# Performance work log

Measured on AMD Instinct MI355X. Metric: run time of the kernel, lower is better.

## Reference

```python
import jax, jax.numpy as jnp
import numpy as np

N_NODES = 5000
N_EDGES = 50000
BATCH = 8
SEQ = 12
IN_CH = 2
HID = 64
OUT_CH = 1
K = 3
N_LAYERS = 2


def setup_inputs() -> dict:
    key = jax.random.key(0)
    ks = jax.random.split(key, 20)
    d = {}
    d["x"] = jax.random.normal(ks[0], (BATCH, SEQ, N_NODES, IN_CH), dtype=jnp.float32)
    d["edge_index"] = jax.random.randint(ks[1], (2, N_EDGES), 0, N_NODES, dtype=jnp.int32)

    def w(k, fin):
        return jax.random.normal(k, (2, K, fin, HID), dtype=jnp.float32) * 0.05

    fins = [IN_CH + HID, HID + HID]
    i = 2
    for l in range(N_LAYERS):
        for g in ("z", "r", "h"):
            d["W" + g + str(l)] = w(ks[i], fins[l]); i += 1
            d["b" + g + str(l)] = jnp.zeros((HID,), jnp.float32)
    d["Wo"] = jax.random.normal(ks[i], (HID, OUT_CH), dtype=jnp.float32) * 0.05
    d["bo"] = jnp.zeros((OUT_CH,), jnp.float32)
    return d


def reference(x, edge_index,
              Wz0, bz0, Wr0, br0, Wh0, bh0,
              Wz1, bz1, Wr1, br1, Wh1, bh1,
              Wo, bo):
    B, T, N, _ = x.shape
    src, dst = edge_index[0], edge_index[1]
    ones = jnp.ones(src.shape, x.dtype)
    deg_out = jax.ops.segment_sum(ones, src, num_segments=N)
    deg_in = jax.ops.segment_sum(ones, dst, num_segments=N)
    inv = lambda dgr: jnp.where(dgr > 0, 1.0 / dgr, 0.0)
    norm_out = inv(deg_out)[src]  # [E], 1/deg_out(src)
    norm_in = inv(deg_in)[dst]    # [E], 1/deg_in(dst)

    def prop(X, norm):
        # X: [N, B, F] -> sparse matvec via gather/scatter
        msg = norm[:, None, None] * X[src]
        return jax.ops.segment_sum(msg, dst, num_segments=N)

    def dconv(X, W, b):
        # X: [N, B, Fin]; W: [2, K, Fin, H]; dual-direction Chebyshev diffusion
        H = jnp.einsum('nbf,fh->nbh', X, W[0, 0] + W[1, 0])
        Tx0o = Tx0i = X
        Tx1o = prop(X, norm_out)
        Tx1i = prop(X, norm_in)
        H = H + jnp.einsum('nbf,fh->nbh', Tx1o, W[0, 1]) \
              + jnp.einsum('nbf,fh->nbh', Tx1i, W[1, 1])
        for k in range(2, W.shape[1]):
            Tx2o = 2.0 * prop(Tx1o, norm_out) - Tx0o
            Tx2i = 2.0 * prop(Tx1i, norm_in) - Tx0i
            H = H + jnp.einsum('nbf,fh->nbh', Tx2o, W[0, k]) \
                  + jnp.einsum('nbf,fh->nbh', Tx2i, W[1, k])
            Tx0o, Tx1o = Tx1o, Tx2o
            Tx0i, Tx1i = Tx1i, Tx2i
        return H + b

    def cell(Xin, H, p):
        Wz, bz, Wr, br, Wh, bh = p
        XH = jnp.concatenate([Xin, H], axis=-1)
        Z = jax.nn.sigmoid(dconv(XH, Wz, bz))
        R = jax.nn.sigmoid(dconv(XH, Wr, br))
        Ht = jnp.tanh(dconv(jnp.concatenate([Xin, H * R], axis=-1), Wh, bh))
        return Z * H + (1.0 - Z) * Ht

    layers = [(Wz0, bz0, Wr0, br0, Wh0, bh0), (Wz1, bz1, Wr1, br1, Wh1, bh1)]
    hid = Wo.shape[0]
    h0 = jnp.zeros((len(layers), N, B, hid), x.dtype)
    xs = jnp.transpose(x, (1, 2, 0, 3))  # [T, N, B, F]

    def step(h, xt):
        inp = xt
        new_h = []
        for l, p in enumerate(layers):
            hl = cell(inp, h[l], p)
            new_h.append(hl)
            inp = hl
        h = jnp.stack(new_h)
        out = jnp.einsum('nbh,ho->nbo', h[-1], Wo) + bo
        return h, out

    _, outs = jax.lax.scan(step, h0, xs)      # [T, N, B, O]
    return jnp.transpose(outs, (2, 0, 1, 3))  # [B, T, N, O]
```

## Files before the change

kernel.cpp:

```cpp
#include <hip/hip_runtime.h>
#include <math.h>

#define NNODES 5000
#define NEDGES 50000
#define SEQT 12
#define NB 40000
#define MAXDEG 128

typedef __attribute__((ext_vector_type(8))) _Float16 half8;
typedef __attribute__((ext_vector_type(2))) _Float16 half2v;
typedef __attribute__((ext_vector_type(4))) float f32x4;


__global__ void count_deg_k(const int* __restrict__ ei, int* deg_out, int* deg_in){
    int e = blockIdx.x*blockDim.x + threadIdx.x;
    if (e < NEDGES){
        atomicAdd(&deg_out[ei[e]], 1);
        atomicAdd(&deg_in[ei[NEDGES + e]], 1);
    }
}

__global__ void scan_k(const int* __restrict__ deg_in, int* __restrict__ row_ptr){
    __shared__ int part[256];
    int tid = threadIdx.x;
    int base = tid*20;
    int loc[20]; int s = 0;
    for (int i=0;i<20;i++){
        int idx = base+i;
        int v = (idx < NNODES) ? deg_in[idx] : 0;
        loc[i] = s; s += v;
    }
    part[tid] = s;
    __syncthreads();
    for (int off=1; off<256; off<<=1){
        int v = (tid>=off) ? part[tid-off] : 0;
        __syncthreads();
        part[tid] += v;
        __syncthreads();
    }
    int prev = (tid==0) ? 0 : part[tid-1];
    for (int i=0;i<20;i++){
        int idx = base+i;
        if (idx < NNODES) row_ptr[idx] = prev + loc[i];
    }
    if (tid==255) row_ptr[NNODES] = part[255];
}

__global__ void fill_csr_k(const int* __restrict__ ei, const int* __restrict__ deg_out,
                           const int* __restrict__ deg_in, const int* __restrict__ row_ptr,
                           int* cursor, int* __restrict__ csr_src,
                           float* __restrict__ csr_wo, float* __restrict__ csr_wi){
    int e = blockIdx.x*blockDim.x + threadIdx.x;
    if (e >= NEDGES) return;
    int s = ei[e], d = ei[NEDGES+e];
    int pos = atomicAdd(&cursor[d], 1);
    int slot = row_ptr[d] + pos;
    csr_src[slot] = s;
    csr_wo[slot] = 1.f/(float)deg_out[s];
    csr_wi[slot] = 1.f/(float)deg_in[d];
}

__global__ void prepack_x_k(const float* __restrict__ x, _Float16* __restrict__ Xtph){
    int idx = blockIdx.x*256 + threadIdx.x;
    if (idx >= SEQT*NB*2) return;
    int tt = idx / (NB*2);
    int r2 = idx - tt*(NB*2);
    int row = r2 >> 1, f = r2 & 1;
    int n = row >> 3, b = row & 7;
    Xtph[idx] = (_Float16)x[((size_t)(b*SEQT+tt)*NNODES + n)*2 + f];
}

__device__ __forceinline__ float wfetch(const float* __restrict__ W, int F, int slot, int f, int c){
    const float* p0 = W + ((size_t)0*F + f)*64 + c;
    const float* p1 = W + ((size_t)1*F + f)*64 + c;
    const float* p2 = W + ((size_t)2*F + f)*64 + c;
    const float* p3 = W + ((size_t)3*F + f)*64 + c;
    const float* p4 = W + ((size_t)4*F + f)*64 + c;
    const float* p5 = W + ((size_t)5*F + f)*64 + c;
    switch(slot){
        case 0: return *p0 + *p3 - *p2 - *p5;
        case 1: return *p1;
        case 2: return *p4;
        case 3: return 2.f * *p2;
        default: return 2.f * *p5;
    }
}

__global__ void pack_l0_k(const float* __restrict__ W, _Float16* __restrict__ wh){
    int idx = blockIdx.x*256 + threadIdx.x;
    if (idx >= 4*11*64) return;
    int lane = idx & 63, rest = idx >> 6;
    int ks = rest % 11, cf = rest / 11;
    int col = cf*16 + (lane & 15);
    int kb = ks*32 + ((lane>>4)<<3);
    size_t o = ((size_t)(ks*4 + cf)*64 + lane)*8;
    for (int j=0;j<8;j++){
        int k = kb + j;
        float v = 0.f;
        if (ks == 0){
            if (k < 10) v = wfetch(W, 66, k>>1, k&1, col);
        } else {
            int slot = (ks-1)>>1;
            int f = 2 + k - 32 - 64*slot;
            v = wfetch(W, 66, slot, f, col);
        }
        wh[o+j] = (_Float16)v;
    }
}

__global__ void pack_l1_k(const float* __restrict__ W, _Float16* __restrict__ wh){
    int idx = blockIdx.x*256 + threadIdx.x;
    if (idx >= 4*20*64) return;
    int lane = idx & 63, rest = idx >> 6;
    int ks = rest % 20, cf = rest / 20;
    int col = cf*16 + (lane & 15);
    int kb = ks*32 + ((lane>>4)<<3);
    int slot = ks >> 2;
    size_t o = ((size_t)(ks*4 + cf)*64 + lane)*8;
    for (int j=0;j<8;j++){
        int k = kb + j;
        int f = k - slot*128;
        wh[o+j] = (_Float16)wfetch(W, 128, slot, f, col);
    }
}


template<int WH>
__global__ __launch_bounds__(WH) void k_dualh(
    const _Float16* __restrict__ S,
    _Float16* __restrict__ Yo, _Float16* __restrict__ Yi,
    const int* __restrict__ rp, const int* __restrict__ cs,
    const float* __restrict__ cwo, const float* __restrict__ cwi){
    constexpr int SLAB = 8*WH;
    int n = blockIdx.x;
    int beg = rp[n], deg = rp[n+1]-beg;
    int nst = deg < MAXDEG ? deg : MAXDEG;
    __shared__ int s_o[MAXDEG]; __shared__ float swo[MAXDEG], swi[MAXDEG];
    for (int j=threadIdx.x; j<nst; j+=WH){
        s_o[j] = cs[beg+j]*SLAB;
        swo[j] = cwo[beg+j]; swi[j] = cwi[beg+j];
    }
    __syncthreads();
    int off = threadIdx.x*8;
    float ao[8] = {0,0,0,0,0,0,0,0}, ai[8] = {0,0,0,0,0,0,0,0};
    for (int j=0;j<nst;j++){
        half8 v = *(const half8*)(S + s_o[j] + off);
        float wo=swo[j], wi=swi[j];
        #pragma unroll
        for (int e=0;e<8;e++){
            float xv = (float)v[e];
            ao[e]=fmaf(wo,xv,ao[e]); ai[e]=fmaf(wi,xv,ai[e]);
        }
    }
    for (int j=nst;j<deg;j++){
        half8 v = *(const half8*)(S + (size_t)cs[beg+j]*SLAB + off);
        float wo=cwo[beg+j], wi=cwi[beg+j];
        #pragma unroll
        for (int e=0;e<8;e++){
            float xv = (float)v[e];
            ao[e]=fmaf(wo,xv,ao[e]); ai[e]=fmaf(wi,xv,ai[e]);
        }
    }
    half8 po, pi;
    #pragma unroll
    for (int e=0;e<8;e++){ po[e]=(_Float16)ao[e]; pi[e]=(_Float16)ai[e]; }
    *(half8*)(Yo + (size_t)n*SLAB + off) = po;
    *(half8*)(Yi + (size_t)n*SLAB + off) = pi;
}

template<int WH>
__global__ __launch_bounds__(WH) void k_prop2h(
    const _Float16* __restrict__ T1o, const _Float16* __restrict__ T1i,
    _Float16* __restrict__ U2o, _Float16* __restrict__ U2i,
    const int* __restrict__ rp, const int* __restrict__ cs,
    const float* __restrict__ cwo, const float* __restrict__ cwi){
    constexpr int SLAB = 8*WH;
    int bx = blockIdx.x;
    int n = bx >> 1, sel = bx & 1;
    const _Float16* S = sel ? T1i : T1o;
    _Float16* U = sel ? U2i : U2o;
    const float* cw = sel ? cwi : cwo;
    int beg = rp[n], deg = rp[n+1]-beg;
    int nst = deg < MAXDEG ? deg : MAXDEG;
    __shared__ int s_o[MAXDEG]; __shared__ float s_w[MAXDEG];
    for (int j=threadIdx.x; j<nst; j+=WH){
        s_o[j] = cs[beg+j]*SLAB;
        s_w[j] = cw[beg+j];
    }
    __syncthreads();
    int off = threadIdx.x*8;
    float a[8] = {0,0,0,0,0,0,0,0};
    for (int j=0;j<nst;j++){
        half8 v = *(const half8*)(S + s_o[j] + off);
        float w=s_w[j];
        #pragma unroll
        for (int e=0;e<8;e++) a[e]=fmaf(w,(float)v[e],a[e]);
    }
    for (int j=nst;j<deg;j++){
        half8 v = *(const half8*)(S + (size_t)cs[beg+j]*SLAB + off);
        float w=cw[beg+j];
        #pragma unroll
        for (int e=0;e<8;e++) a[e]=fmaf(w,(float)v[e],a[e]);
    }
    half8 p;
    #pragma unroll
    for (int e=0;e<8;e++) p[e]=(_Float16)a[e];
    *(half8*)(U + (size_t)n*SLAB + off) = p;
}

__global__ __launch_bounds__(64) void k_dual_l0zrh(
    const _Float16* __restrict__ h0h, const _Float16* __restrict__ Xt,
    _Float16* __restrict__ T1o, _Float16* __restrict__ T1i, _Float16* __restrict__ XTh,
    const int* __restrict__ rp, const int* __restrict__ cs,
    const float* __restrict__ cwo, const float* __restrict__ cwi){
    int n = blockIdx.x;
    int beg = rp[n], deg = rp[n+1]-beg;
    int nst = deg < MAXDEG ? deg : MAXDEG;
    __shared__ int s_o[MAXDEG]; __shared__ float swo[MAXDEG], swi[MAXDEG];
    for (int j=threadIdx.x; j<nst; j+=64){
        s_o[j] = cs[beg+j]*512;
        swo[j] = cwo[beg+j]; swi[j] = cwi[beg+j];
    }
    __syncthreads();
    int off = threadIdx.x*8;
    {
        float ao[8] = {0,0,0,0,0,0,0,0}, ai[8] = {0,0,0,0,0,0,0,0};
        for (int j=0;j<nst;j++){
            half8 v = *(const half8*)(h0h + s_o[j] + off);
            float wo=swo[j], wi=swi[j];
            #pragma unroll
            for (int e=0;e<8;e++){
                float xv = (float)v[e];
                ao[e]=fmaf(wo,xv,ao[e]); ai[e]=fmaf(wi,xv,ai[e]);
            }
        }
        for (int j=nst;j<deg;j++){
            half8 v = *(const half8*)(h0h + (size_t)cs[beg+j]*512 + off);
            float wo=cwo[beg+j], wi=cwi[beg+j];
            #pragma unroll
            for (int e=0;e<8;e++){
                float xv = (float)v[e];
                ao[e]=fmaf(wo,xv,ao[e]); ai[e]=fmaf(wi,xv,ai[e]);
            }
        }
        half8 po, pi;
        #pragma unroll
        for (int e=0;e<8;e++){ po[e]=(_Float16)ao[e]; pi[e]=(_Float16)ai[e]; }
        *(half8*)(T1o + (size_t)n*512 + off) = po;
        *(half8*)(T1i + (size_t)n*512 + off) = pi;
    }
    if (threadIdx.x < 8){
        int b = threadIdx.x;
        float ax0=0,ax1=0, ay0=0,ay1=0;
        for (int j=0;j<nst;j++){
            int src = s_o[j] >> 9;
            half2v v = *(const half2v*)(Xt + src*16 + b*2);
            float x0=(float)v[0], x1=(float)v[1];
            ax0=fmaf(swo[j],x0,ax0); ax1=fmaf(swo[j],x1,ax1);
            ay0=fmaf(swi[j],x0,ay0); ay1=fmaf(swi[j],x1,ay1);
        }
        for (int j=nst;j<deg;j++){
            int src = cs[beg+j];
            half2v v = *(const half2v*)(Xt + src*16 + b*2);
            float x0=(float)v[0], x1=(float)v[1];
            ax0=fmaf(cwo[beg+j],x0,ax0); ax1=fmaf(cwo[beg+j],x1,ax1);
            ay0=fmaf(cwi[beg+j],x0,ay0); ay1=fmaf(cwi[beg+j],x1,ay1);
        }
        size_t ro = (size_t)(n*8 + b)*32;
        XTh[ro+0] = Xt[(size_t)(n*8+b)*2+0];
        XTh[ro+1] = Xt[(size_t)(n*8+b)*2+1];
        XTh[ro+2] = (_Float16)ax0; XTh[ro+3] = (_Float16)ax1;
        XTh[ro+4] = (_Float16)ay0; XTh[ro+5] = (_Float16)ay1;
    }
}

__global__ __launch_bounds__(64) void k_prop2_l0zrh(
    const _Float16* __restrict__ T1o, const _Float16* __restrict__ T1i,
    _Float16* __restrict__ T2o, _Float16* __restrict__ T2i, _Float16* __restrict__ XTh,
    const int* __restrict__ rp, const int* __restrict__ cs,
    const float* __restrict__ cwo, const float* __restrict__ cwi){
    int bx = blockIdx.x;
    int n = bx >> 1, sel = bx & 1;
    const _Float16* S = sel ? T1i : T1o;
    _Float16* U = sel ? T2i : T2o;
    const float* cw = sel ? cwi : cwo;
    int beg = rp[n], deg = rp[n+1]-beg;
    int nst = deg < MAXDEG ? deg : MAXDEG;
    __shared__ int s_o[MAXDEG]; __shared__ float s_w[MAXDEG];
    for (int j=threadIdx.x; j<nst; j+=64){
        s_o[j] = cs[beg+j]*512;
        s_w[j] = cw[beg+j];
    }
    __syncthreads();
    int off = threadIdx.x*8;
    {
        float a[8] = {0,0,0,0,0,0,0,0};
        for (int j=0;j<nst;j++){
            half8 v = *(const half8*)(S + s_o[j] + off);
            float w=s_w[j];
            #pragma unroll
            for (int e=0;e<8;e++) a[e]=fmaf(w,(float)v[e],a[e]);
        }
        for (int j=nst;j<deg;j++){
            half8 v = *(const half8*)(S + (size_t)cs[beg+j]*512 + off);
            float w=cw[beg+j];
            #pragma unroll
            for (int e=0;e<8;e++) a[e]=fmaf(w,(float)v[e],a[e]);
        }
        half8 p;
        #pragma unroll
        for (int e=0;e<8;e++) p[e]=(_Float16)a[e];
        *(half8*)(U + (size_t)n*512 + off) = p;
    }
    if (threadIdx.x < 8){
        int b = threadIdx.x;
        int xo = 2 + 2*sel;
        float a0=0,a1=0;
        for (int j=0;j<nst;j++){
            int src = s_o[j] >> 9;
            half2v v = *(const half2v*)(XTh + (size_t)src*256 + b*32 + xo);
            a0=fmaf(s_w[j],(float)v[0],a0); a1=fmaf(s_w[j],(float)v[1],a1);
        }
        for (int j=nst;j<deg;j++){
            int src = cs[beg+j];
            half2v v = *(const half2v*)(XTh + (size_t)src*256 + b*32 + xo);
            a0=fmaf(cw[beg+j],(float)v[0],a0); a1=fmaf(cw[beg+j],(float)v[1],a1);
        }
        size_t ro = (size_t)(n*8 + b)*32 + 6 + 2*sel;
        XTh[ro+0] = (_Float16)a0; XTh[ro+1] = (_Float16)a1;
    }
}

__global__ __launch_bounds__(128) void k_dual2x64h(
    const _Float16* __restrict__ h0h, const _Float16* __restrict__ h1h,
    _Float16* __restrict__ T1o, _Float16* __restrict__ T1i,
    const int* __restrict__ rp, const int* __restrict__ cs,
    const float* __restrict__ cwo, const float* __restrict__ cwi){
    int n = blockIdx.x;
    int beg = rp[n], deg = rp[n+1]-beg;
    int nst = deg < MAXDEG ? deg : MAXDEG;
    __shared__ int s_o[MAXDEG]; __shared__ float swo[MAXDEG], swi[MAXDEG];
    for (int j=threadIdx.x; j<nst; j+=128){
        s_o[j] = cs[beg+j]*512;
        swo[j] = cwo[beg+j]; swi[j] = cwi[beg+j];
    }
    __syncthreads();
    int off = threadIdx.x*8;
    int b = off >> 7, c = off & 127;
    const _Float16* S = (c < 64) ? h0h : h1h;
    int soff = b*64 + (c & 63);
    float ao[8] = {0,0,0,0,0,0,0,0}, ai[8] = {0,0,0,0,0,0,0,0};
    for (int j=0;j<nst;j++){
        half8 v = *(const half8*)(S + s_o[j] + soff);
        float wo=swo[j], wi=swi[j];
        #pragma unroll
        for (int e=0;e<8;e++){
            float xv = (float)v[e];
            ao[e]=fmaf(wo,xv,ao[e]); ai[e]=fmaf(wi,xv,ai[e]);
        }
    }
    for (int j=nst;j<deg;j++){
        half8 v = *(const half8*)(S + (size_t)cs[beg+j]*512 + soff);
        float wo=cwo[beg+j], wi=cwi[beg+j];
        #pragma unroll
        for (int e=0;e<8;e++){
            float xv = (float)v[e];
            ao[e]=fmaf(wo,xv,ao[e]); ai[e]=fmaf(wi,xv,ai[e]);
        }
    }
    half8 po, pi;
    #pragma unroll
    for (int e=0;e<8;e++){ po[e]=(_Float16)ao[e]; pi[e]=(_Float16)ai[e]; }
    *(half8*)(T1o + (size_t)n*1024 + off) = po;
    *(half8*)(T1i + (size_t)n*1024 + off) = pi;
}


struct KD { const _Float16* a; int st; };
struct GA { KD kd[20]; };

template<int NK, int NG, int EPI>
__global__ __launch_bounds__(256) void k_gemm(GA ga,
    const _Float16* __restrict__ wh0, const float* __restrict__ b0,
    const _Float16* __restrict__ wh1, const float* __restrict__ b1,
    float* __restrict__ Z, _Float16* __restrict__ Gout,
    float* __restrict__ Hf, _Float16* __restrict__ Hh,
    const float* __restrict__ Wo, const float* __restrict__ bo,
    float* __restrict__ out, int t){
    __shared__ _Float16 ldsb[2][NG*2048];
    __shared__ float spr[4][32];
    const int tid = threadIdx.x;
    const int lane = tid & 63, wv = tid >> 6, rl = lane & 15, kg = lane >> 4;
    const int m0 = blockIdx.x*64 + (wv&1)*32;
    const int cfb = (wv>>1)*2;
    const _Float16* wsrc[2] = {wh0, wh1};

    half8 srg[NG];
    half8 a0, a1, a0n, a1n;

    auto sload = [&](int ks){
        #pragma unroll
        for (int j=0;j<NG;j++)
            srg[j] = *(const half8*)(wsrc[j] + (size_t)ks*2048 + tid*8);
    };
    auto swrite = [&](int buf){
        #pragma unroll
        for (int j=0;j<NG;j++)
            *(half8*)&ldsb[buf][j*2048 + tid*8] = srg[j];
    };
    auto aload = [&](int ks, half8& x0, half8& x1){
        const _Float16* base = ga.kd[ks].a;
        const int st = ga.kd[ks].st;
        x0 = *(const half8*)(base + (size_t)(m0+rl)*st + kg*8);
        x1 = *(const half8*)(base + (size_t)(m0+16+rl)*st + kg*8);
    };

    f32x4 acc[NG][2][2];
    #pragma unroll
    for (int g=0; g<NG; ++g)
        #pragma unroll
        for (int cc=0; cc<2; ++cc)
            #pragma unroll
            for (int mr=0; mr<2; ++mr){
                acc[g][cc][mr][0]=0.f; acc[g][cc][mr][1]=0.f;
                acc[g][cc][mr][2]=0.f; acc[g][cc][mr][3]=0.f;
            }

    sload(0); swrite(0);
    if (NK>1) sload(1);
    aload(0, a0, a1);
    __syncthreads();
    for (int ks=0; ks<NK; ++ks){
        const int cur = ks & 1;
        if (ks+1 < NK){ swrite(cur^1); aload(ks+1, a0n, a1n); }
        if (ks+2 < NK) sload(ks+2);
        #pragma unroll
        for (int g=0; g<NG; ++g){
            #pragma unroll
            for (int cc=0; cc<2; ++cc){
                half8 bv = *(const half8*)&ldsb[cur][g*2048 + (cfb+cc)*512 + lane*8];
                acc[g][cc][0] = __builtin_amdgcn_mfma_f32_16x16x32_f16(a0, bv, acc[g][cc][0], 0, 0, 0);
                acc[g][cc][1] = __builtin_amdgcn_mfma_f32_16x16x32_f16(a1, bv, acc[g][cc][1], 0, 0, 0);
            }
        }
        __syncthreads();
        a0 = a0n; a1 = a1n;
    }

    if constexpr (EPI == 0){
        #pragma unroll
        for (int cc=0; cc<2; ++cc){
            const int col = (cfb+cc)*16 + rl;
            float bzv = b0[col], brv = b1[col];
            #pragma unroll
            for (int mr=0; mr<2; ++mr)
                #pragma unroll
                for (int i=0;i<4;i++){
                    int row = m0 + mr*16 + kg*4 + i;
                    float z = 1.f/(1.f+__expf(-(acc[0][cc][mr][i] + bzv)));
                    float r = 1.f/(1.f+__expf(-(acc[NG-1][cc][mr][i] + brv)));
                    size_t ix = (size_t)row*64 + col;
                    Z[ix] = z;
                    Gout[ix] = (_Float16)(Hf[ix]*r);
                }
        }
    } else {
        float pr[2][4] = {{0.f,0.f,0.f,0.f},{0.f,0.f,0.f,0.f}};
        #pragma unroll
        for (int cc=0; cc<2; ++cc){
            const int col = (cfb+cc)*16 + rl;
            float bv = b0[col];
            float wo_c = 0.f;
            if constexpr (EPI == 2) wo_c = Wo[col];
            #pragma unroll
            for (int mr=0; mr<2; ++mr)
                #pragma unroll
                for (int i=0;i<4;i++){
                    int row = m0 + mr*16 + kg*4 + i;
                    float ht = tanhf(acc[0][cc][mr][i] + bv);
                    size_t ix = (size_t)row*64 + col;
                    float z = Z[ix];
                    float hn = z*Hf[ix] + (1.f-z)*ht;
                    Hf[ix] = hn;
                    Hh[ix] = (_Float16)hn;
                    if constexpr (EPI == 2) pr[mr][i] = fmaf(hn, wo_c, pr[mr][i]);
                }
        }
        if constexpr (EPI == 2){
            #pragma unroll
            for (int mr=0; mr<2; ++mr)
                #pragma unroll
                for (int i=0;i<4;i++){
                    float v = pr[mr][i];
                    v += __shfl_xor(v, 1);
                    v += __shfl_xor(v, 2);
                    v += __shfl_xor(v, 4);
                    v += __shfl_xor(v, 8);
                    if (rl == 0) spr[wv][mr*16 + kg*4 + i] = v;
                }
            __syncthreads();
            if (tid < 64){
                int r = tid;
                float v = spr[r>>5][r&31] + spr[(r>>5)|2][r&31] + bo[0];
                int row = blockIdx.x*64 + r;
                int n = row >> 3, b = row & 7;
                out[(size_t)(b*SEQT + t)*NNODES + n] = v;
            }
        }
    }
}


extern "C" void kernel_launch(void* const* d_in, const int* in_sizes, int n_in,
                              void* d_out, int out_size, void* d_ws, size_t ws_size,
                              hipStream_t stream){
    (void)in_sizes; (void)n_in; (void)out_size; (void)ws_size;
    const float* x  = (const float*)d_in[0];
    const int*   ei = (const int*)d_in[1];
    const float* Wz[2] = {(const float*)d_in[2],  (const float*)d_in[8]};
    const float* bz[2] = {(const float*)d_in[3],  (const float*)d_in[9]};
    const float* Wr[2] = {(const float*)d_in[4],  (const float*)d_in[10]};
    const float* br[2] = {(const float*)d_in[5],  (const float*)d_in[11]};
    const float* Wh[2] = {(const float*)d_in[6],  (const float*)d_in[12]};
    const float* bh[2] = {(const float*)d_in[7],  (const float*)d_in[13]};
    const float* Wo = (const float*)d_in[14];
    const float* bo = (const float*)d_in[15];
    float* out = (float*)d_out;

    char* p = (char*)d_ws;
    auto alloc = [&](size_t bytes)->char*{
        char* r = p; p += (bytes + 255) & ~(size_t)255; return r;
    };
    const size_t H64  = (size_t)NB*64*2;
    const size_t H128 = (size_t)NB*128*2;
    const size_t F64  = (size_t)NB*64*4;

    _Float16* Xtph = (_Float16*)alloc((size_t)SEQT*NB*2*2);
    float*    h0f = (float*)alloc(F64);
    float*    h1f = (float*)alloc(F64);
    float*    Z0  = (float*)alloc(F64);
    float*    Z1  = (float*)alloc(F64);
    _Float16* h0h = (_Float16*)alloc(H64);
    _Float16* h1h = (_Float16*)alloc(H64);
    _Float16* XTh = (_Float16*)alloc((size_t)NB*32*2);
    _Float16* Th1o = (_Float16*)alloc(H64);
    _Float16* Th1i = (_Float16*)alloc(H64);
    _Float16* Th2o = (_Float16*)alloc(H64);
    _Float16* Th2i = (_Float16*)alloc(H64);
    _Float16* G0L0 = (_Float16*)alloc(H64);
    _Float16* G1o0 = (_Float16*)alloc(H64);
    _Float16* G1i0 = (_Float16*)alloc(H64);
    _Float16* G2o0 = (_Float16*)alloc(H64);
    _Float16* G2i0 = (_Float16*)alloc(H64);
    _Float16* T1o128 = (_Float16*)alloc(H128);
    _Float16* T1i128 = (_Float16*)alloc(H128);
    _Float16* U2o128 = (_Float16*)alloc(H128);
    _Float16* U2i128 = (_Float16*)alloc(H128);
    _Float16* G0p  = (_Float16*)alloc(H64);
    _Float16* G1o1 = (_Float16*)alloc(H64);
    _Float16* G1i1 = (_Float16*)alloc(H64);
    _Float16* G2o1 = (_Float16*)alloc(H64);
    _Float16* G2i1 = (_Float16*)alloc(H64);
    _Float16 *whl0[3], *whl1[3];
    for (int g=0; g<3; ++g){
        whl0[g] = (_Float16*)alloc((size_t)4*11*64*8*2);
        whl1[g] = (_Float16*)alloc((size_t)4*20*64*8*2);
    }
    int* deg_out = (int*)alloc(NNODES*4);
    int* deg_in  = (int*)alloc(NNODES*4);
    int* row_ptr = (int*)alloc((NNODES+1)*4);
    int* cursor  = (int*)alloc(NNODES*4);
    int* csr_src = (int*)alloc(NEDGES*4);
    float* csr_wo = (float*)alloc(NEDGES*4);
    float* csr_wi = (float*)alloc(NEDGES*4);

    hipMemsetAsync(deg_out, 0, NNODES*4, stream);
    hipMemsetAsync(deg_in,  0, NNODES*4, stream);
    hipMemsetAsync(cursor,  0, NNODES*4, stream);
    hipMemsetAsync(h0f, 0, F64, stream);
    hipMemsetAsync(h1f, 0, F64, stream);
    hipMemsetAsync(h0h, 0, H64, stream);
    hipMemsetAsync(h1h, 0, H64, stream);
    hipMemsetAsync(XTh, 0, (size_t)NB*32*2, stream);

    count_deg_k<<<(NEDGES+255)/256, 256, 0, stream>>>(ei, deg_out, deg_in);
    scan_k<<<1, 256, 0, stream>>>(deg_in, row_ptr);
    fill_csr_k<<<(NEDGES+255)/256, 256, 0, stream>>>(ei, deg_out, deg_in, row_ptr,
                                                     cursor, csr_src, csr_wo, csr_wi);
    prepack_x_k<<<(SEQT*NB*2+255)/256, 256, 0, stream>>>(x, Xtph);
    const float* Wptr0[3] = {Wz[0], Wr[0], Wh[0]};
    const float* Wptr1[3] = {Wz[1], Wr[1], Wh[1]};
    for (int g=0; g<3; ++g){
        pack_l0_k<<<(4*11*64+255)/256, 256, 0, stream>>>(Wptr0[g], whl0[g]);
        pack_l1_k<<<(4*20*64+255)/256, 256, 0, stream>>>(Wptr1[g], whl1[g]);
    }

    GA gaL0zr = {}, gaL0h = {}, gaL1zr = {}, gaL1h = {};
    {
        const _Float16* t64[5] = {h0h, Th1o, Th1i, Th2o, Th2i};
        gaL0zr.kd[0] = {XTh, 32};
        for (int s=0; s<5; ++s){
            gaL0zr.kd[1+2*s] = {t64[s], 64};
            gaL0zr.kd[2+2*s] = {t64[s]+32, 64};
        }
        const _Float16* g64[5] = {G0L0, G1o0, G1i0, G2o0, G2i0};
        gaL0h.kd[0] = {XTh, 32};
        for (int s=0; s<5; ++s){
            gaL0h.kd[1+2*s] = {g64[s], 64};
            gaL0h.kd[2+2*s] = {g64[s]+32, 64};
        }
        gaL1zr.kd[0] = {h0h, 64};    gaL1zr.kd[1] = {h0h+32, 64};
        gaL1zr.kd[2] = {h1h, 64};    gaL1zr.kd[3] = {h1h+32, 64};
        const _Float16* t128[4] = {T1o128, T1i128, U2o128, U2i128};
        for (int s=0; s<4; ++s)
            for (int q=0; q<4; ++q)
                gaL1zr.kd[4+4*s+q] = {t128[s]+32*q, 128};
        gaL1h.kd[0] = {h0h, 64};  gaL1h.kd[1] = {h0h+32, 64};
        gaL1h.kd[2] = {G0p, 64};  gaL1h.kd[3] = {G0p+32, 64};
        const _Float16* gh[4] = {G1o1, G1i1, G2o1, G2i1};
        for (int s=0; s<4; ++s){
            gaL1h.kd[4+4*s+0] = {t128[s], 128};
            gaL1h.kd[4+4*s+1] = {t128[s]+32, 128};
            gaL1h.kd[4+4*s+2] = {gh[s], 64};
            gaL1h.kd[4+4*s+3] = {gh[s]+32, 64};
        }
    }

    for (int t=0; t<SEQT; ++t){
        k_dual_l0zrh<<<NNODES, 64, 0, stream>>>(h0h, Xtph + (size_t)t*NB*2, Th1o, Th1i, XTh,
                                                row_ptr, csr_src, csr_wo, csr_wi);
        k_prop2_l0zrh<<<2*NNODES, 64, 0, stream>>>(Th1o, Th1i, Th2o, Th2i, XTh,
                                                row_ptr, csr_src, csr_wo, csr_wi);
        k_gemm<11,2,0><<<NB/64, 256, 0, stream>>>(gaL0zr,
            whl0[0], bz[0], whl0[1], br[0],
            Z0, G0L0, h0f, nullptr, nullptr, nullptr, nullptr, 0);
        k_dualh<64><<<NNODES, 64, 0, stream>>>(G0L0, G1o0, G1i0, row_ptr, csr_src, csr_wo, csr_wi);
        k_prop2h<64><<<2*NNODES, 64, 0, stream>>>(G1o0, G1i0, G2o0, G2i0,
                                                row_ptr, csr_src, csr_wo, csr_wi);
        k_gemm<11,1,1><<<NB/64, 256, 0, stream>>>(gaL0h,
            whl0[2], bh[0], nullptr, nullptr,
            Z0, nullptr, h0f, h0h, nullptr, nullptr, nullptr, 0);
        k_dual2x64h<<<NNODES, 128, 0, stream>>>(h0h, h1h, T1o128, T1i128,
                                                row_ptr, csr_src, csr_wo, csr_wi);
        k_prop2h<128><<<2*NNODES, 128, 0, stream>>>(T1o128, T1i128, U2o128, U2i128,
                                                row_ptr, csr_src, csr_wo, csr_wi);
        k_gemm<20,2,0><<<NB/64, 256, 0, stream>>>(gaL1zr,
            whl1[0], bz[1], whl1[1], br[1],
            Z1, G0p, h1f, nullptr, nullptr, nullptr, nullptr, 0);
        k_dualh<64><<<NNODES, 64, 0, stream>>>(G0p, G1o1, G1i1, row_ptr, csr_src, csr_wo, csr_wi);
        k_prop2h<64><<<2*NNODES, 64, 0, stream>>>(G1o1, G1i1, G2o1, G2i1,
                                                row_ptr, csr_src, csr_wo, csr_wi);
        k_gemm<20,1,2><<<NB/64, 256, 0, stream>>>(gaL1h,
            whl1[2], bh[1], nullptr, nullptr,
            Z1, nullptr, h1f, h1h, Wo, bo, out, t);
    }
}
```

Before: 2.409 ms.

## Unroll gather loops, merge dual-direction prop blocks, deepen GEMM A-prefetch queue

The sparse gather loops in the diffusion kernels are unrolled by four so several neighbour loads are in flight at once. The second-hop propagation kernels now run the out and in directions in one block of twice the width, so CSR indices and weights are staged into shared memory once per node instead of twice. The MFMA GEMM replaces its single-stage A-operand prefetch with a four-deep register queue to hide global load latency. The deeper queue and unrolling raise register pressure, which may reduce occupancy.

```diff
diff --git a/kernel.cpp b/kernel.cpp
--- a/kernel.cpp
+++ b/kernel.cpp
@@ -125,6 +125,16 @@
 }
 
 
+#define ACC8(vv, ww) { \
+    float _w = (ww); \
+    _Pragma("unroll") \
+    for (int e=0;e<8;e++) a[e]=fmaf(_w,(float)(vv)[e],a[e]); }
+#define ACC8D(vv, wo_, wi_) { \
+    float _wo = (wo_), _wi = (wi_); \
+    _Pragma("unroll") \
+    for (int e=0;e<8;e++){ float xv=(float)(vv)[e]; \
+        ao[e]=fmaf(_wo,xv,ao[e]); ai[e]=fmaf(_wi,xv,ai[e]); } }
+
 template<int WH>
 __global__ __launch_bounds__(WH) void k_dualh(
     const _Float16* __restrict__ S,
@@ -143,23 +153,24 @@
     __syncthreads();
     int off = threadIdx.x*8;
     float ao[8] = {0,0,0,0,0,0,0,0}, ai[8] = {0,0,0,0,0,0,0,0};
-    for (int j=0;j<nst;j++){
+    int j = 0;
+    for (; j+3<nst; j+=4){
+        half8 v0 = *(const half8*)(S + s_o[j]   + off);
+        half8 v1 = *(const half8*)(S + s_o[j+1] + off);
+        half8 v2 = *(const half8*)(S + s_o[j+2] + off);
+        half8 v3 = *(const half8*)(S + s_o[j+3] + off);
+        ACC8D(v0, swo[j],   swi[j]);
+        ACC8D(v1, swo[j+1], swi[j+1]);
+        ACC8D(v2, swo[j+2], swi[j+2]);
+        ACC8D(v3, swo[j+3], swi[j+3]);
+    }
+    for (; j<nst; ++j){
         half8 v = *(const half8*)(S + s_o[j] + off);
-        float wo=swo[j], wi=swi[j];
-        #pragma unroll
-        for (int e=0;e<8;e++){
-            float xv = (float)v[e];
-            ao[e]=fmaf(wo,xv,ao[e]); ai[e]=fmaf(wi,xv,ai[e]);
-        }
-    }
-    for (int j=nst;j<deg;j++){
+        ACC8D(v, swo[j], swi[j]);
+    }
+    for (j=nst; j<deg; ++j){
         half8 v = *(const half8*)(S + (size_t)cs[beg+j]*SLAB + off);
-        float wo=cwo[beg+j], wi=cwi[beg+j];
-        #pragma unroll
-        for (int e=0;e<8;e++){
-            float xv = (float)v[e];
-            ao[e]=fmaf(wo,xv,ao[e]); ai[e]=fmaf(wi,xv,ai[e]);
-        }
+        ACC8D(v, cwo[beg+j], cwi[beg+j]);
     }
     half8 po, pi;
     #pragma unroll
@@ -169,38 +180,42 @@
 }
 
 template<int WH>
-__global__ __launch_bounds__(WH) void k_prop2h(
+__global__ __launch_bounds__(2*WH) void k_prop2m(
     const _Float16* __restrict__ T1o, const _Float16* __restrict__ T1i,
     _Float16* __restrict__ U2o, _Float16* __restrict__ U2i,
     const int* __restrict__ rp, const int* __restrict__ cs,
     const float* __restrict__ cwo, const float* __restrict__ cwi){
     constexpr int SLAB = 8*WH;
-    int bx = blockIdx.x;
-    int n = bx >> 1, sel = bx & 1;
+    int n = blockIdx.x;
+    int beg = rp[n], deg = rp[n+1]-beg;
+    int nst = deg < MAXDEG ? deg : MAXDEG;
+    __shared__ int s_o[MAXDEG]; __shared__ float swo[MAXDEG], swi[MAXDEG];
+    for (int j=threadIdx.x; j<nst; j+=2*WH){
+        s_o[j] = cs[beg+j]*SLAB;
+        swo[j] = cwo[beg+j]; swi[j] = cwi[beg+j];
+    }
+    __syncthreads();
+    const int sel = (threadIdx.x >= WH);
     const _Float16* S = sel ? T1i : T1o;
     _Float16* U = sel ? U2i : U2o;
-    const float* cw = sel ? cwi : cwo;
-    int beg = rp[n], deg = rp[n+1]-beg;
-    int nst = deg < MAXDEG ? deg : MAXDEG;
-    __shared__ int s_o[MAXDEG]; __shared__ float s_w[MAXDEG];
-    for (int j=threadIdx.x; j<nst; j+=WH){
-        s_o[j] = cs[beg+j]*SLAB;
-        s_w[j] = cw[beg+j];
-    }
-    __syncthreads();
-    int off = threadIdx.x*8;
+    const float* sw = sel ? swi : swo;
+    int off = (threadIdx.x & (WH-1))*8;
     float a[8] = {0,0,0,0,0,0,0,0};
-    for (int j=0;j<nst;j++){
+    int j = 0;
+    for (; j+3<nst; j+=4){
+        half8 v0 = *(const half8*)(S + s_o[j]   + off);
+        half8 v1 = *(const half8*)(S + s_o[j+1] + off);
+        half8 v2 = *(const half8*)(S + s_o[j+2] + off);
+        half8 v3 = *(const half8*)(S + s_o[j+3] + off);
+        ACC8(v0, sw[j]); ACC8(v1, sw[j+1]); ACC8(v2, sw[j+2]); ACC8(v3, sw[j+3]);
+    }
+    for (; j<nst; ++j){
         half8 v = *(const half8*)(S + s_o[j] + off);
-        float w=s_w[j];
-        #pragma unroll
-        for (int e=0;e<8;e++) a[e]=fmaf(w,(float)v[e],a[e]);
-    }
-    for (int j=nst;j<deg;j++){
+        ACC8(v, sw[j]);
+    }
+    for (j=nst; j<deg; ++j){
         half8 v = *(const half8*)(S + (size_t)cs[beg+j]*SLAB + off);
-        float w=cw[beg+j];
-        #pragma unroll
-        for (int e=0;e<8;e++) a[e]=fmaf(w,(float)v[e],a[e]);
+        ACC8(v, sel ? cwi[beg+j] : cwo[beg+j]);
     }
     half8 p;
     #pragma unroll
@@ -225,23 +240,24 @@
     int off = threadIdx.x*8;
     {
         float ao[8] = {0,0,0,0,0,0,0,0}, ai[8] = {0,0,0,0,0,0,0,0};
-        for (int j=0;j<nst;j++){
+        int j = 0;
+        for (; j+3<nst; j+=4){
+            half8 v0 = *(const half8*)(h0h + s_o[j]   + off);
+            half8 v1 = *(const half8*)(h0h + s_o[j+1] + off);
+            half8 v2 = *(const half8*)(h0h + s_o[j+2] + off);
+            half8 v3 = *(const half8*)(h0h + s_o[j+3] + off);
+            ACC8D(v0, swo[j],   swi[j]);
+            ACC8D(v1, swo[j+1], swi[j+1]);
+            ACC8D(v2, swo[j+2], swi[j+2]);
+            ACC8D(v3, swo[j+3], swi[j+3]);
+        }
+        for (; j<nst; ++j){
             half8 v = *(const half8*)(h0h + s_o[j] + off);
-            float wo=swo[j], wi=swi[j];
-            #pragma unroll
-            for (int e=0;e<8;e++){
-                float xv = (float)v[e];
-                ao[e]=fmaf(wo,xv,ao[e]); ai[e]=fmaf(wi,xv,ai[e]);
-            }
-        }
-        for (int j=nst;j<deg;j++){
+            ACC8D(v, swo[j], swi[j]);
+        }
+        for (j=nst; j<deg; ++j){
             half8 v = *(const half8*)(h0h + (size_t)cs[beg+j]*512 + off);
-            float wo=cwo[beg+j], wi=cwi[beg+j];
-            #pragma unroll
-            for (int e=0;e<8;e++){
-                float xv = (float)v[e];
-                ao[e]=fmaf(wo,xv,ao[e]); ai[e]=fmaf(wi,xv,ai[e]);
-            }
+            ACC8D(v, cwo[beg+j], cwi[beg+j]);
         }
         half8 po, pi;
         #pragma unroll
@@ -274,57 +290,62 @@
     }
 }
 
-__global__ __launch_bounds__(64) void k_prop2_l0zrh(
+__global__ __launch_bounds__(128) void k_prop2_l0m(
     const _Float16* __restrict__ T1o, const _Float16* __restrict__ T1i,
     _Float16* __restrict__ T2o, _Float16* __restrict__ T2i, _Float16* __restrict__ XTh,
     const int* __restrict__ rp, const int* __restrict__ cs,
     const float* __restrict__ cwo, const float* __restrict__ cwi){
-    int bx = blockIdx.x;
-    int n = bx >> 1, sel = bx & 1;
+    int n = blockIdx.x;
+    int beg = rp[n], deg = rp[n+1]-beg;
+    int nst = deg < MAXDEG ? deg : MAXDEG;
+    __shared__ int s_o[MAXDEG]; __shared__ float swo[MAXDEG], swi[MAXDEG];
+    for (int j=threadIdx.x; j<nst; j+=128){
+        s_o[j] = cs[beg+j]*512;
+        swo[j] = cwo[beg+j]; swi[j] = cwi[beg+j];
+    }
+    __syncthreads();
+    const int sel = (threadIdx.x >= 64);
     const _Float16* S = sel ? T1i : T1o;
     _Float16* U = sel ? T2i : T2o;
-    const float* cw = sel ? cwi : cwo;
-    int beg = rp[n], deg = rp[n+1]-beg;
-    int nst = deg < MAXDEG ? deg : MAXDEG;
-    __shared__ int s_o[MAXDEG]; __shared__ float s_w[MAXDEG];
-    for (int j=threadIdx.x; j<nst; j+=64){
-        s_o[j] = cs[beg+j]*512;
-        s_w[j] = cw[beg+j];
-    }
-    __syncthreads();
-    int off = threadIdx.x*8;
+    const float* sw = sel ? swi : swo;
+    int off = (threadIdx.x & 63)*8;
     {
         float a[8] = {0,0,0,0,0,0,0,0};
-        for (int j=0;j<nst;j++){
+        int j = 0;
+        for (; j+3<nst; j+=4){
+            half8 v0 = *(const half8*)(S + s_o[j]   + off);
+            half8 v1 = *(const half8*)(S + s_o[j+1] + off);
+            half8 v2 = *(const half8*)(S + s_o[j+2] + off);
+            half8 v3 = *(const half8*)(S + s_o[j+3] + off);
+            ACC8(v0, sw[j]); ACC8(v1, sw[j+1]); ACC8(v2, sw[j+2]); ACC8(v3, sw[j+3]);
+        }
+        for (; j<nst; ++j){
             half8 v = *(const half8*)(S + s_o[j] + off);
-            float w=s_w[j];
-            #pragma unroll
-            for (int e=0;e<8;e++) a[e]=fmaf(w,(float)v[e],a[e]);
-        }
-        for (int j=nst;j<deg;j++){
+            ACC8(v, sw[j]);
+        }
+        for (j=nst; j<deg; ++j){
             half8 v = *(const half8*)(S + (size_t)cs[beg+j]*512 + off);
-            float w=cw[beg+j];
-            #pragma unroll
-            for (int e=0;e<8;e++) a[e]=fmaf(w,(float)v[e],a[e]);
+            ACC8(v, sel ? cwi[beg+j] : cwo[beg+j]);
         }
         half8 p;
         #pragma unroll
         for (int e=0;e<8;e++) p[e]=(_Float16)a[e];
         *(half8*)(U + (size_t)n*512 + off) = p;
     }
-    if (threadIdx.x < 8){
-        int b = threadIdx.x;
+    if ((threadIdx.x & 63) < 8){
+        int b = threadIdx.x & 7;
         int xo = 2 + 2*sel;
         float a0=0,a1=0;
         for (int j=0;j<nst;j++){
             int src = s_o[j] >> 9;
             half2v v = *(const half2v*)(XTh + (size_t)src*256 + b*32 + xo);
-            a0=fmaf(s_w[j],(float)v[0],a0); a1=fmaf(s_w[j],(float)v[1],a1);
+            a0=fmaf(sw[j],(float)v[0],a0); a1=fmaf(sw[j],(float)v[1],a1);
         }
         for (int j=nst;j<deg;j++){
             int src = cs[beg+j];
+            float w = sel ? cwi[beg+j] : cwo[beg+j];
             half2v v = *(const half2v*)(XTh + (size_t)src*256 + b*32 + xo);
-            a0=fmaf(cw[beg+j],(float)v[0],a0); a1=fmaf(cw[beg+j],(float)v[1],a1);
+            a0=fmaf(w,(float)v[0],a0); a1=fmaf(w,(float)v[1],a1);
         }
         size_t ro = (size_t)(n*8 + b)*32 + 6 + 2*sel;
         XTh[ro+0] = (_Float16)a0; XTh[ro+1] = (_Float16)a1;
@@ -350,23 +371,24 @@
     const _Float16* S = (c < 64) ? h0h : h1h;
     int soff = b*64 + (c & 63);
     float ao[8] = {0,0,0,0,0,0,0,0}, ai[8] = {0,0,0,0,0,0,0,0};
-    for (int j=0;j<nst;j++){
+    int j = 0;
+    for (; j+3<nst; j+=4){
+        half8 v0 = *(const half8*)(S + s_o[j]   + soff);
+        half8 v1 = *(const half8*)(S + s_o[j+1] + soff);
+        half8 v2 = *(const half8*)(S + s_o[j+2] + soff);
+        half8 v3 = *(const half8*)(S + s_o[j+3] + soff);
+        ACC8D(v0, swo[j],   swi[j]);
+        ACC8D(v1, swo[j+1], swi[j+1]);
+        ACC8D(v2, swo[j+2], swi[j+2]);
+        ACC8D(v3, swo[j+3], swi[j+3]);
+    }
+    for (; j<nst; ++j){
         half8 v = *(const half8*)(S + s_o[j] + soff);
-        float wo=swo[j], wi=swi[j];
-        #pragma unroll
-        for (int e=0;e<8;e++){
-            float xv = (float)v[e];
-            ao[e]=fmaf(wo,xv,ao[e]); ai[e]=fmaf(wi,xv,ai[e]);
-        }
-    }
-    for (int j=nst;j<deg;j++){
+        ACC8D(v, swo[j], swi[j]);
+    }
+    for (j=nst; j<deg; ++j){
         half8 v = *(const half8*)(S + (size_t)cs[beg+j]*512 + soff);
-        float wo=cwo[beg+j], wi=cwi[beg+j];
-        #pragma unroll
-        for (int e=0;e<8;e++){
-            float xv = (float)v[e];
-            ao[e]=fmaf(wo,xv,ao[e]); ai[e]=fmaf(wi,xv,ai[e]);
-        }
+        ACC8D(v, cwo[beg+j], cwi[beg+j]);
     }
     half8 po, pi;
     #pragma unroll
@@ -387,6 +409,7 @@
     float* __restrict__ Hf, _Float16* __restrict__ Hh,
     const float* __restrict__ Wo, const float* __restrict__ bo,
     float* __restrict__ out, int t){
+    constexpr int QD = 4;
     __shared__ _Float16 ldsb[2][NG*2048];
     __shared__ float spr[4][32];
     const int tid = threadIdx.x;
@@ -396,8 +419,6 @@
     const _Float16* wsrc[2] = {wh0, wh1};
 
     half8 srg[NG];
-    half8 a0, a1, a0n, a1n;
-
     auto sload = [&](int ks){
         #pragma unroll
         for (int j=0;j<NG;j++)
@@ -426,14 +447,20 @@
                 acc[g][cc][mr][2]=0.f; acc[g][cc][mr][3]=0.f;
             }
 
+    half8 aq0[QD], aq1[QD];
+    #pragma unroll
+    for (int i=0; i<QD && i<NK; ++i) aload(i, aq0[i], aq1[i]);
     sload(0); swrite(0);
     if (NK>1) sload(1);
-    aload(0, a0, a1);
     __syncthreads();
+    #pragma unroll
     for (int ks=0; ks<NK; ++ks){
         const int cur = ks & 1;
-        if (ks+1 < NK){ swrite(cur^1); aload(ks+1, a0n, a1n); }
+        const int qs = ks % QD;
+        half8 a0 = aq0[qs], a1 = aq1[qs];
+        if (ks+1 < NK) swrite(cur^1);
         if (ks+2 < NK) sload(ks+2);
+        if (ks+QD < NK) aload(ks+QD, aq0[qs], aq1[qs]);
         #pragma unroll
         for (int g=0; g<NG; ++g){
             #pragma unroll
@@ -444,7 +471,6 @@
             }
         }
         __syncthreads();
-        a0 = a0n; a1 = a1n;
     }
 
     if constexpr (EPI == 0){
@@ -629,26 +655,26 @@
     for (int t=0; t<SEQT; ++t){
         k_dual_l0zrh<<<NNODES, 64, 0, stream>>>(h0h, Xtph + (size_t)t*NB*2, Th1o, Th1i, XTh,
                                                 row_ptr, csr_src, csr_wo, csr_wi);
-        k_prop2_l0zrh<<<2*NNODES, 64, 0, stream>>>(Th1o, Th1i, Th2o, Th2i, XTh,
+        k_prop2_l0m<<<NNODES, 128, 0, stream>>>(Th1o, Th1i, Th2o, Th2i, XTh,
                                                 row_ptr, csr_src, csr_wo, csr_wi);
         k_gemm<11,2,0><<<NB/64, 256, 0, stream>>>(gaL0zr,
             whl0[0], bz[0], whl0[1], br[0],
             Z0, G0L0, h0f, nullptr, nullptr, nullptr, nullptr, 0);
         k_dualh<64><<<NNODES, 64, 0, stream>>>(G0L0, G1o0, G1i0, row_ptr, csr_src, csr_wo, csr_wi);
-        k_prop2h<64><<<2*NNODES, 64, 0, stream>>>(G1o0, G1i0, G2o0, G2i0,
+        k_prop2m<64><<<NNODES, 128, 0, stream>>>(G1o0, G1i0, G2o0, G2i0,
                                                 row_ptr, csr_src, csr_wo, csr_wi);
         k_gemm<11,1,1><<<NB/64, 256, 0, stream>>>(gaL0h,
             whl0[2], bh[0], nullptr, nullptr,
             Z0, nullptr, h0f, h0h, nullptr, nullptr, nullptr, 0);
         k_dual2x64h<<<NNODES, 128, 0, stream>>>(h0h, h1h, T1o128, T1i128,
                                                 row_ptr, csr_src, csr_wo, csr_wi);
-        k_prop2h<128><<<2*NNODES, 128, 0, stream>>>(T1o128, T1i128, U2o128, U2i128,
+        k_prop2m<128><<<NNODES, 256, 0, stream>>>(T1o128, T1i128, U2o128, U2i128,
                                                 row_ptr, csr_src, csr_wo, csr_wi);
         k_gemm<20,2,0><<<NB/64, 256, 0, stream>>>(gaL1zr,
             whl1[0], bz[1], whl1[1], br[1],
             Z1, G0p, h1f, nullptr, nullptr, nullptr, nullptr, 0);
         k_dualh<64><<<NNODES, 64, 0, stream>>>(G0p, G1o1, G1i1, row_ptr, csr_src, csr_wo, csr_wi);
-        k_prop2h<64><<<2*NNODES, 64, 0, stream>>>(G1o1, G1i1, G2o1, G2i1,
+        k_prop2m<64><<<NNODES, 128, 0, stream>>>(G1o1, G1i1, G2o1, G2i1,
                                                 row_ptr, csr_src, csr_wo, csr_wi);
         k_gemm<20,1,2><<<NB/64, 256, 0, stream>>>(gaL1h,
             whl1[2], bh[1], nullptr, nullptr,
```

Result: slower. 2.517 ms (+4.5%).
